# Kernel optimization log

Measured on AMD Instinct MI355X. Metric: run time of the kernel, lower is better.

Reference implementation:

```python
import jax, jax.numpy as jnp
import numpy as np

L = 3          # num_layers
D = 512        # hidden_dim
B, N = 8, 1024
EPS = 1e-5


def layernorm(x, gamma, beta):
    mu = jnp.mean(x, axis=-1, keepdims=True)
    var = jnp.var(x, axis=-1, keepdims=True)
    return (x - mu) * jax.lax.rsqrt(var + EPS) * gamma + beta


def setup_inputs() -> dict:
    key = jax.random.key(0)
    ks = jax.random.split(key, 12)
    s = 1.0 / np.sqrt(D)
    node_features = jax.random.normal(ks[0], (B, N, D), dtype=jnp.float32)
    adjacency_matrix = jax.random.randint(ks[1], (B, N, N), 0, 2, dtype=jnp.int32)
    return {
        "node_features": node_features,
        "adjacency_matrix": adjacency_matrix,
        # attn_linear: Linear(2D, 1) -> weight [2D], bias scalar, per layer
        "attn_w": jax.random.normal(ks[2], (L, 2 * D), dtype=jnp.float32) * (1.0 / np.sqrt(2 * D)),
        "attn_b": jax.random.normal(ks[3], (L,), dtype=jnp.float32) * 0.01,
        "W1": jax.random.normal(ks[4], (L, D, 4 * D), dtype=jnp.float32) * s,
        "b1": jnp.zeros((L, 4 * D), dtype=jnp.float32),
        "W2": jax.random.normal(ks[5], (L, 4 * D, D), dtype=jnp.float32) * (1.0 / np.sqrt(4 * D)),
        "b2": jnp.zeros((L, D), dtype=jnp.float32),
        "g1": jnp.ones((L, D), dtype=jnp.float32),
        "beta1": jnp.zeros((L, D), dtype=jnp.float32),
        "g2": jnp.ones((L, D), dtype=jnp.float32),
        "beta2": jnp.zeros((L, D), dtype=jnp.float32),
    }


def reference(node_features, adjacency_matrix, attn_w, attn_b, W1, b1, W2, b2, g1, beta1, g2, beta2):
    n = adjacency_matrix.shape[-1]
    # adjacency + self loops; mask of allowed edges
    mask = (adjacency_matrix.astype(jnp.float32) + jnp.eye(n, dtype=jnp.float32)) > 0  # [B,N,N]
    x = node_features
    d = x.shape[-1]
    for l in range(attn_w.shape[0]):
        # score_ij = a1.h_i + a2.h_j + b  (== Linear(concat(h_i,h_j)))
        si = x @ attn_w[l, :d]           # [B,N]
        sj = x @ attn_w[l, d:]           # [B,N]
        scores = si[:, :, None] + sj[:, None, :] + attn_b[l]   # [B,N,N]
        scores = jnp.where(scores >= 0, scores, 0.2 * scores)  # LeakyReLU(0.2)
        scores = jnp.where(mask, scores, -jnp.inf)
        attn = jax.nn.softmax(scores, axis=-1)                  # diag always unmasked
        agg = jnp.einsum('bij,bjd->bid', attn, x)
        h = layernorm(x + agg, g1[l], beta1[l])
        ff = jax.nn.gelu(h @ W1[l] + b1[l], approximate=False) @ W2[l] + b2[l]
        x = layernorm(h + ff, g2[l], beta2[l])
    return x
```

## Files before the change

### kernel.cpp

```cpp
#include <hip/hip_runtime.h>
#include <math.h>

#define NB 8
#define NN 1024
#define DD 512

typedef unsigned short u16;
typedef unsigned int u32;
typedef unsigned long long u64;
typedef __attribute__((ext_vector_type(8))) short bfrag;
typedef __attribute__((ext_vector_type(4))) float ffrag;

__device__ __forceinline__ u16 f2b(float f) {
    union { float f; u32 u; } v; v.f = f;
    u32 r = v.u + 0x7fffu + ((v.u >> 16) & 1u);
    return (u16)(r >> 16);
}
__device__ __forceinline__ float b2f(u16 b) {
    union { u32 u; float f; } v; v.u = ((u32)b) << 16;
    return v.f;
}

__device__ __forceinline__ float gelu_cheap(float v) {
    float s = v * 0.70710678118654752f;
    float a = fabsf(s);
    float t = 1.0f / (1.0f + 0.3275911f * a);
    float p = ((((1.061405429f * t - 1.453152027f) * t + 1.421413741f) * t
                - 0.284496736f) * t + 0.254829592f) * t;
    float erfa = 1.0f - p * __expf(-a * a);
    float erfs = copysignf(erfa, s);
    return 0.5f * v * (1.0f + erfs);
}

__device__ __forceinline__ void gload_lds16(const void* g, void* l) {
    __builtin_amdgcn_global_load_lds(
        (const __attribute__((address_space(1))) void*)g,
        (__attribute__((address_space(3))) void*)l, 16, 0, 0);
}

__global__ __launch_bounds__(256) void mask_pack(const int* __restrict__ adj,
                                                 u64* __restrict__ mb) {
    int idx = blockIdx.x * 256 + threadIdx.x;
    int w = idx & 15;
    int bi = idx >> 4;
    int i = bi & 1023;
    const int4* p = (const int4*)(adj + (size_t)bi * NN + w * 64);
    u64 m = 0;
#pragma unroll
    for (int q = 0; q < 16; ++q) {
        int4 v = p[q];
        if (v.x > 0) m |= 1ull << (q * 4 + 0);
        if (v.y > 0) m |= 1ull << (q * 4 + 1);
        if (v.z > 0) m |= 1ull << (q * 4 + 2);
        if (v.w > 0) m |= 1ull << (q * 4 + 3);
    }
    if (w == (i >> 6)) m |= 1ull << (i & 63);
    mb[idx] = m;
}

__global__ __launch_bounds__(256) void transpose_cvt(
    const float* __restrict__ in, u16* __restrict__ out,
    int R, int C, size_t inStr, size_t outStr)
{
    __shared__ float tile[32][33];
    int z = blockIdx.z;
    int r0 = blockIdx.y * 32, c0 = blockIdx.x * 32;
    int t = threadIdx.x;
    int tr = t >> 3, tc = (t & 7) * 4;
    float4 v = *(const float4*)(in + inStr * z + (size_t)(r0 + tr) * C + c0 + tc);
    tile[tr][tc + 0] = v.x; tile[tr][tc + 1] = v.y;
    tile[tr][tc + 2] = v.z; tile[tr][tc + 3] = v.w;
    __syncthreads();
    u32 w0 = (u32)f2b(tile[tc + 0][tr]) | ((u32)f2b(tile[tc + 1][tr]) << 16);
    u32 w1 = (u32)f2b(tile[tc + 2][tr]) | ((u32)f2b(tile[tc + 3][tr]) << 16);
    uint2 wv; wv.x = w0; wv.y = w1;
    *(uint2*)(out + outStr * z + (size_t)(c0 + tr) * R + r0 + tc) = wv;
}

__global__ __launch_bounds__(256) void score_proj_kernel(
    const float* __restrict__ x, const float* __restrict__ w,
    float* __restrict__ si, float* __restrict__ sj)
{
    int wave = threadIdx.x >> 6;
    int lane = threadIdx.x & 63;
    int row = blockIdx.x * 4 + wave;
    const float4* xr = (const float4*)(x + (size_t)row * DD) + lane * 2;
    const float4* w1 = (const float4*)(w) + lane * 2;
    const float4* w2 = (const float4*)(w + DD) + lane * 2;
    float a = 0.f, b2 = 0.f;
#pragma unroll
    for (int c = 0; c < 2; ++c) {
        float4 xv = xr[c], wa = w1[c], wb = w2[c];
        a  += xv.x * wa.x + xv.y * wa.y + xv.z * wa.z + xv.w * wa.w;
        b2 += xv.x * wb.x + xv.y * wb.y + xv.z * wb.z + xv.w * wb.w;
    }
#pragma unroll
    for (int off = 32; off > 0; off >>= 1) {
        a  += __shfl_xor(a, off);
        b2 += __shfl_xor(b2, off);
    }
    if (lane == 0) { si[row] = a; sj[row] = b2; }
}

__global__ __launch_bounds__(256) void softmax_p(
    const float* __restrict__ si, const float* __restrict__ sj,
    const float* __restrict__ attn_b, const u64* __restrict__ mb,
    u16* __restrict__ P)
{
    __shared__ u16 sb[8 * NN];
    int b  = blockIdx.x >> 7;
    int i0 = (blockIdx.x & 127) * 8;
    int tid = threadIdx.x;
    int r = tid >> 5, l32 = tid & 31;
    int i = i0 + r;
    float bb = attn_b[0];
    float siv = si[b * NN + i];
    const float* sjb = sj + b * NN;
    const u64* mbr = mb + ((size_t)b * NN + i) * 16;

    float sv[32];
    float mx = -INFINITY;
#pragma unroll
    for (int q = 0; q < 32; ++q) {
        int j = q * 32 + l32;
        u64 w = mbr[q >> 1];
        int bit = ((q & 1) << 5) + l32;
        float s = siv + sjb[j] + bb;
        s = (s >= 0.f) ? s : 0.2f * s;
        s = ((w >> bit) & 1ull) ? s : -INFINITY;
        sv[q] = s;
        mx = fmaxf(mx, s);
    }
#pragma unroll
    for (int off = 16; off > 0; off >>= 1) mx = fmaxf(mx, __shfl_xor(mx, off, 32));
    float sum = 0.f;
#pragma unroll
    for (int q = 0; q < 32; ++q) {
        float p = __expf(sv[q] - mx);
        sv[q] = p;
        sum += p;
    }
#pragma unroll
    for (int off = 16; off > 0; off >>= 1) sum += __shfl_xor(sum, off, 32);
    float inv = 1.f / sum;
#pragma unroll
    for (int q = 0; q < 32; ++q)
        sb[r * NN + q * 32 + l32] = f2b(sv[q] * inv);
    __syncthreads();
    const uint4* src = (const uint4*)sb;
    uint4* dst = (uint4*)(P + ((size_t)b * NN + i0) * NN);
#pragma unroll
    for (int t = 0; t < 4; ++t) dst[t * 256 + tid] = src[t * 256 + tid];
}

template <int EPI>
__global__ __launch_bounds__(256) void gemm64(
    const u16* __restrict__ A, const u16* __restrict__ Bm,
    const float* __restrict__ bias, const void* __restrict__ res,
    void* __restrict__ Cout, int K, int N, int lda, int ldb,
    size_t aStr, size_t bStr, size_t cStr, size_t resStr)
{
    __shared__ __align__(16) u16 lds[24576];
    int z = blockIdx.z;
    int m0 = blockIdx.y * 64, n0 = blockIdx.x * 128;
    int tid = threadIdx.x;
    int lane = tid & 63, wv = tid >> 6;

    const u16* ag[2]; const u16* bg[4];
    u32 la[2], lb[4];
#pragma unroll
    for (int i = 0; i < 2; ++i) {
        int q = i * 256 + tid;
        int row = q >> 3, c = q & 7;
        ag[i] = A + aStr * z + (size_t)(m0 + row) * lda + (c ^ (row & 7)) * 8;
        la[i] = i * 2048 + wv * 512;
    }
#pragma unroll
    for (int i = 0; i < 4; ++i) {
        int q = i * 256 + tid;
        int row = q >> 3, c = q & 7;
        bg[i] = Bm + bStr * z + (size_t)(n0 + row) * ldb + (c ^ (row & 7)) * 8;
        lb[i] = 8192 + i * 2048 + wv * 512;
    }

    int mw = (wv >> 1) * 32, nw = (wv & 1) * 64;
    int lr = lane & 15, lq = lane >> 4;
    int sw = lr & 7;

    ffrag acc[2][4];
#pragma unroll
    for (int i = 0; i < 2; ++i)
#pragma unroll
        for (int j = 0; j < 4; ++j) acc[i][j] = (ffrag){0.f, 0.f, 0.f, 0.f};

#pragma unroll
    for (int i = 0; i < 2; ++i) gload_lds16(ag[i], &lds[la[i]]);
#pragma unroll
    for (int i = 0; i < 4; ++i) gload_lds16(bg[i], &lds[lb[i]]);

    for (int k0 = 0; k0 < K; k0 += 64) {
        int cur = (k0 >> 6) & 1;
        if (k0 + 64 < K) {
#pragma unroll
            for (int i = 0; i < 2; ++i)
                gload_lds16(ag[i] + k0 + 64, &lds[((cur ^ 1) << 12) + la[i]]);
#pragma unroll
            for (int i = 0; i < 4; ++i)
                gload_lds16(bg[i] + k0 + 64, &lds[((cur ^ 1) << 13) + lb[i]]);
            asm volatile("s_waitcnt vmcnt(6)" ::: "memory");
        } else {
            asm volatile("s_waitcnt vmcnt(0)" ::: "memory");
        }
        asm volatile("s_barrier" ::: "memory");

        const u16* Ab = &lds[cur << 12];
        const u16* Bb = &lds[8192 + (cur << 13)];
#pragma unroll
        for (int h = 0; h < 2; ++h) {
            bfrag af[2], bf[4];
#pragma unroll
            for (int i = 0; i < 2; ++i)
                af[i] = *(const bfrag*)&Ab[(mw + i * 16 + lr) * 64 + ((h * 4 + lq) ^ sw) * 8];
#pragma unroll
            for (int j = 0; j < 4; ++j)
                bf[j] = *(const bfrag*)&Bb[(nw + j * 16 + lr) * 64 + ((h * 4 + lq) ^ sw) * 8];
#pragma unroll
            for (int i = 0; i < 2; ++i)
#pragma unroll
                for (int j = 0; j < 4; ++j)
                    acc[i][j] = __builtin_amdgcn_mfma_f32_16x16x32_bf16(af[i], bf[j], acc[i][j], 0, 0, 0);
        }
        asm volatile("s_waitcnt lgkmcnt(0)\ns_barrier" ::: "memory");
    }

    float* Cf = (float*)Cout + cStr * z;
    u16*   Cb = (u16*)Cout + cStr * z;
    const float* resf = (const float*)res;
    const u16*   resb = (const u16*)res;
#pragma unroll
    for (int i = 0; i < 2; ++i) {
        int row = m0 + mw + i * 16 + lq * 4;
#pragma unroll
        for (int j = 0; j < 4; ++j) {
            int col = n0 + nw + j * 16 + lr;
            float bv = (EPI != 0) ? bias[col] : 0.f;
#pragma unroll
            for (int r = 0; r < 4; ++r) {
                float v = acc[i][j][r] + bv;
                size_t off = (size_t)(row + r) * N + col;
                if (EPI == 1) {
                    Cb[off] = f2b(gelu_cheap(v));
                } else if (EPI == 0) {
                    Cf[off] = v + resf[resStr * z + off];
                } else {
                    Cf[off] = v + b2f(resb[off]);
                }
            }
        }
    }
}

template <int EPI>
__global__ __launch_bounds__(256) void gemm128(
    const u16* __restrict__ A, const u16* __restrict__ Bm,
    const float* __restrict__ bias, const void* __restrict__ res,
    void* __restrict__ Cout, int K, int N, int lda, int ldb,
    size_t aStr, size_t bStr, size_t cStr, size_t resStr)
{
    __shared__ __align__(16) u16 lds[32768];
    int z = blockIdx.z;
    int m0 = blockIdx.y * 128, n0 = blockIdx.x * 128;
    int tid = threadIdx.x;
    int lane = tid & 63, wv = tid >> 6;

    const u16* ag[4]; const u16* bg[4];
    u32 la[4], lb[4];
#pragma unroll
    for (int i = 0; i < 4; ++i) {
        int q = i * 256 + tid;
        int row = q >> 3, c = q & 7;
        ag[i] = A + aStr * z + (size_t)(m0 + row) * lda + (c ^ (row & 7)) * 8;
        la[i] = i * 2048 + wv * 512;
        bg[i] = Bm + bStr * z + (size_t)(n0 + row) * ldb + (c ^ (row & 7)) * 8;
        lb[i] = 16384 + i * 2048 + wv * 512;
    }

    int mw = (wv >> 1) * 64, nw = (wv & 1) * 64;
    int lr = lane & 15, lq = lane >> 4;
    int sw = lr & 7;

    ffrag acc[4][4];
#pragma unroll
    for (int i = 0; i < 4; ++i)
#pragma unroll
        for (int j = 0; j < 4; ++j) acc[i][j] = (ffrag){0.f, 0.f, 0.f, 0.f};

#pragma unroll
    for (int i = 0; i < 4; ++i) gload_lds16(ag[i], &lds[la[i]]);
#pragma unroll
    for (int i = 0; i < 4; ++i) gload_lds16(bg[i], &lds[lb[i]]);

    for (int k0 = 0; k0 < K; k0 += 64) {
        int cur = (k0 >> 6) & 1;
        if (k0 + 64 < K) {
#pragma unroll
            for (int i = 0; i < 4; ++i)
                gload_lds16(ag[i] + k0 + 64, &lds[((cur ^ 1) << 13) + la[i]]);
#pragma unroll
            for (int i = 0; i < 4; ++i)
                gload_lds16(bg[i] + k0 + 64, &lds[((cur ^ 1) << 13) + lb[i]]);
            asm volatile("s_waitcnt vmcnt(8)" ::: "memory");
        } else {
            asm volatile("s_waitcnt vmcnt(0)" ::: "memory");
        }
        asm volatile("s_barrier" ::: "memory");

        const u16* Ab = &lds[cur << 13];
        const u16* Bb = &lds[16384 + (cur << 13)];
#pragma unroll
        for (int h = 0; h < 2; ++h) {
            bfrag af[4], bf[4];
#pragma unroll
            for (int i = 0; i < 4; ++i)
                af[i] = *(const bfrag*)&Ab[(mw + i * 16 + lr) * 64 + ((h * 4 + lq) ^ sw) * 8];
#pragma unroll
            for (int j = 0; j < 4; ++j)
                bf[j] = *(const bfrag*)&Bb[(nw + j * 16 + lr) * 64 + ((h * 4 + lq) ^ sw) * 8];
#pragma unroll
            for (int i = 0; i < 4; ++i)
#pragma unroll
                for (int j = 0; j < 4; ++j)
                    acc[i][j] = __builtin_amdgcn_mfma_f32_16x16x32_bf16(af[i], bf[j], acc[i][j], 0, 0, 0);
        }
        asm volatile("s_waitcnt lgkmcnt(0)\ns_barrier" ::: "memory");
    }

    float* Cf = (float*)Cout + cStr * z;
    u16*   Cb = (u16*)Cout + cStr * z;
    const float* resf = (const float*)res;
    const u16*   resb = (const u16*)res;
#pragma unroll
    for (int i = 0; i < 4; ++i) {
        int row = m0 + mw + i * 16 + lq * 4;
#pragma unroll
        for (int j = 0; j < 4; ++j) {
            int col = n0 + nw + j * 16 + lr;
            float bv = (EPI != 0) ? bias[col] : 0.f;
#pragma unroll
            for (int r = 0; r < 4; ++r) {
                float v = acc[i][j][r] + bv;
                size_t off = (size_t)(row + r) * N + col;
                if (EPI == 1) {
                    Cb[off] = f2b(gelu_cheap(v));
                } else if (EPI == 0) {
                    Cf[off] = v + resf[resStr * z + off];
                } else {
                    Cf[off] = v + b2f(resb[off]);
                }
            }
        }
    }
}

template <bool BF, bool SP>
__global__ __launch_bounds__(256) void ln_kernel(
    const float* __restrict__ in, const float* __restrict__ g,
    const float* __restrict__ be, void* __restrict__ out,
    const float* __restrict__ aw, float* __restrict__ si, float* __restrict__ sj)
{
    int row = blockIdx.x;
    int tid = threadIdx.x;
    const float2* rp = (const float2*)(in + (size_t)row * DD);
    float2 v = rp[tid];
    float s  = v.x + v.y;
    float ss = v.x * v.x + v.y * v.y;
#pragma unroll
    for (int off = 32; off > 0; off >>= 1) {
        s  += __shfl_xor(s, off);
        ss += __shfl_xor(ss, off);
    }
    __shared__ float sh[8];
    int wave = tid >> 6, lane = tid & 63;
    if (lane == 0) { sh[wave] = s; sh[4 + wave] = ss; }
    __syncthreads();
    float S  = sh[0] + sh[1] + sh[2] + sh[3];
    float SS = sh[4] + sh[5] + sh[6] + sh[7];
    float mean = S * (1.f / DD);
    float var  = SS * (1.f / DD) - mean * mean;
    var = fmaxf(var, 0.f);
    float rs = rsqrtf(var + 1e-5f);
    float2 gv = ((const float2*)g)[tid];
    float2 bv = ((const float2*)be)[tid];
    float ox = (v.x - mean) * rs * gv.x + bv.x;
    float oy = (v.y - mean) * rs * gv.y + bv.y;
    if (BF) {
        u32 w = (u32)f2b(ox) | ((u32)f2b(oy) << 16);
        ((u32*)out)[(size_t)row * (DD / 2) + tid] = w;
    } else {
        float2 o; o.x = ox; o.y = oy;
        ((float2*)out)[(size_t)row * (DD / 2) + tid] = o;
    }
    if (SP) {
        float2 wa = ((const float2*)aw)[tid];
        float2 wb = ((const float2*)(aw + DD))[tid];
        float a = ox * wa.x + oy * wa.y;
        float c = ox * wb.x + oy * wb.y;
#pragma unroll
        for (int off = 32; off > 0; off >>= 1) {
            a += __shfl_xor(a, off);
            c += __shfl_xor(c, off);
        }
        __syncthreads();
        if (lane == 0) { sh[wave] = a; sh[4 + wave] = c; }
        __syncthreads();
        if (tid == 0) {
            si[row] = sh[0] + sh[1] + sh[2] + sh[3];
            sj[row] = sh[4] + sh[5] + sh[6] + sh[7];
        }
    }
}

extern "C" void kernel_launch(void* const* d_in, const int* in_sizes, int n_in,
                              void* d_out, int out_size, void* d_ws, size_t ws_size,
                              hipStream_t stream) {
    const float* nf     = (const float*)d_in[0];
    const int*   adj    = (const int*)d_in[1];
    const float* attn_w = (const float*)d_in[2];
    const float* attn_b = (const float*)d_in[3];
    const float* W1     = (const float*)d_in[4];
    const float* b1     = (const float*)d_in[5];
    const float* W2     = (const float*)d_in[6];
    const float* b2     = (const float*)d_in[7];
    const float* g1     = (const float*)d_in[8];
    const float* be1    = (const float*)d_in[9];
    const float* g2     = (const float*)d_in[10];
    const float* be2    = (const float*)d_in[11];
    float* out = (float*)d_out;

    char* wsb = (char*)d_ws;
    float* x_cur = (float*)(wsb);
    u16*   h_bf  = (u16*)(wsb + 16777216);
    char*  scr   = wsb + 25165824;
    u16*   P     = (u16*)scr;
    float* hres  = (float*)(scr + 16777216);
    u16*   mid   = (u16*)scr;
    u16*   xT    = (u16*)(wsb + 58720256);
    u16*   W1t   = (u16*)(wsb + 67108864);
    u16*   W2t   = (u16*)(wsb + 73400320);
    u64*   mask  = (u64*)(wsb + 79691776);
    float* si    = (float*)(wsb + 80740352);
    float* sj    = (float*)(wsb + 80773120);

    mask_pack<<<512, 256, 0, stream>>>(adj, mask);
    transpose_cvt<<<dim3(64, 16, 3), 256, 0, stream>>>(W1, W1t, 512, 2048,
                                                       (size_t)512 * 2048, (size_t)512 * 2048);
    transpose_cvt<<<dim3(16, 64, 3), 256, 0, stream>>>(W2, W2t, 2048, 512,
                                                       (size_t)2048 * 512, (size_t)2048 * 512);

    score_proj_kernel<<<2048, 256, 0, stream>>>(nf, attn_w, si, sj);

    for (int l = 0; l < 3; ++l) {
        const float* xin = (l == 0) ? nf : x_cur;
        transpose_cvt<<<dim3(16, 32, 8), 256, 0, stream>>>(xin, xT, 1024, 512,
                                                           (size_t)NN * DD, (size_t)NN * DD);
        softmax_p<<<1024, 256, 0, stream>>>(si, sj, attn_b + l, mask, P);
        gemm64<0><<<dim3(4, 16, 8), 256, 0, stream>>>(
            P, xT, nullptr, xin, hres, 1024, 512, 1024, 1024,
            (size_t)NN * NN, (size_t)DD * NN, (size_t)NN * DD, (size_t)NN * DD);
        ln_kernel<true, false><<<8192, 256, 0, stream>>>(
            hres, g1 + (size_t)l * 512, be1 + (size_t)l * 512, h_bf, nullptr, nullptr, nullptr);
        gemm128<1><<<dim3(16, 64, 1), 256, 0, stream>>>(
            h_bf, W1t + (size_t)l * 1048576, b1 + (size_t)l * 2048, nullptr, mid,
            512, 2048, 512, 512, 0, 0, 0, 0);
        gemm64<2><<<dim3(4, 128, 1), 256, 0, stream>>>(
            mid, W2t + (size_t)l * 1048576, b2 + (size_t)l * 512, h_bf, x_cur,
            2048, 512, 2048, 2048, 0, 0, 0, 0);
        if (l < 2) {
            ln_kernel<false, true><<<8192, 256, 0, stream>>>(
                x_cur, g2 + (size_t)l * 512, be2 + (size_t)l * 512, x_cur,
                attn_w + (size_t)(l + 1) * 1024, si, sj);
        } else {
            ln_kernel<false, false><<<8192, 256, 0, stream>>>(
                x_cur, g2 + (size_t)l * 512, be2 + (size_t)l * 512, out,
                nullptr, nullptr, nullptr);
        }
    }
}
```

Measured before the change: 476.0 us.

## Remap GEMM workgroups across XCDs and stage GELU epilogue stores through LDS

Both GEMM kernels now remap the linear workgroup index so that consecutive tiles land on the same XCD (stride-8 interleave), which should improve L2 reuse of shared A/B panels on the chiplet GPU. The GELU epilogue of gemm128 writes bf16 results into LDS with a padded stride, then copies them out as coalesced 16-byte row stores instead of scattered 2-byte stores. The remap assumes the workgroup count is divisible by 8, and the LDS staging adds a barrier.

```diff
diff --git a/kernel.cpp b/kernel.cpp
--- a/kernel.cpp
+++ b/kernel.cpp
@@ -161,8 +161,14 @@
     size_t aStr, size_t bStr, size_t cStr, size_t resStr)
 {
     __shared__ __align__(16) u16 lds[24576];
-    int z = blockIdx.z;
-    int m0 = blockIdx.y * 64, n0 = blockIdx.x * 128;
+    int gx = gridDim.x, gy = gridDim.y;
+    int wg = blockIdx.x + gx * (blockIdx.y + gy * blockIdx.z);
+    int nwg = gx * gy * gridDim.z;
+    wg = (wg & 7) * (nwg >> 3) + (wg >> 3);
+    int z = wg / (gx * gy);
+    int rem = wg - z * (gx * gy);
+    int by = rem / gx, bx = rem - by * gx;
+    int m0 = by * 64, n0 = bx * 128;
     int tid = threadIdx.x;
     int lane = tid & 63, wv = tid >> 6;
 
@@ -268,8 +274,14 @@
     size_t aStr, size_t bStr, size_t cStr, size_t resStr)
 {
     __shared__ __align__(16) u16 lds[32768];
-    int z = blockIdx.z;
-    int m0 = blockIdx.y * 128, n0 = blockIdx.x * 128;
+    int gx = gridDim.x, gy = gridDim.y;
+    int wg = blockIdx.x + gx * (blockIdx.y + gy * blockIdx.z);
+    int nwg = gx * gy * gridDim.z;
+    wg = (wg & 7) * (nwg >> 3) + (wg >> 3);
+    int z = wg / (gx * gy);
+    int rem = wg - z * (gx * gy);
+    int by = rem / gx, bx = rem - by * gx;
+    int m0 = by * 128, n0 = bx * 128;
     int tid = threadIdx.x;
     int lane = tid & 63, wv = tid >> 6;
 
@@ -339,23 +351,46 @@
     u16*   Cb = (u16*)Cout + cStr * z;
     const float* resf = (const float*)res;
     const u16*   resb = (const u16*)res;
-#pragma unroll
-    for (int i = 0; i < 4; ++i) {
-        int row = m0 + mw + i * 16 + lq * 4;
-#pragma unroll
-        for (int j = 0; j < 4; ++j) {
-            int col = n0 + nw + j * 16 + lr;
-            float bv = (EPI != 0) ? bias[col] : 0.f;
-#pragma unroll
-            for (int r = 0; r < 4; ++r) {
-                float v = acc[i][j][r] + bv;
-                size_t off = (size_t)(row + r) * N + col;
-                if (EPI == 1) {
-                    Cb[off] = f2b(gelu_cheap(v));
-                } else if (EPI == 0) {
-                    Cf[off] = v + resf[resStr * z + off];
-                } else {
-                    Cf[off] = v + b2f(resb[off]);
+    if (EPI == 1) {
+        u16* sb = lds;
+#pragma unroll
+        for (int i = 0; i < 4; ++i) {
+            int rr = mw + i * 16 + lq * 4;
+#pragma unroll
+            for (int j = 0; j < 4; ++j) {
+                int cc = nw + j * 16 + lr;
+                float bv = bias[n0 + cc];
+#pragma unroll
+                for (int r = 0; r < 4; ++r)
+                    sb[(rr + r) * 136 + cc] = f2b(gelu_cheap(acc[i][j][r] + bv));
+            }
+        }
+        __syncthreads();
+        u16* Crow = Cb + (size_t)m0 * N + n0;
+#pragma unroll
+        for (int t = 0; t < 8; ++t) {
+            int q = t * 256 + tid;
+            int row = q >> 4, c16 = q & 15;
+            *(uint4*)(Crow + (size_t)row * N + c16 * 8) =
+                *(const uint4*)(sb + row * 136 + c16 * 8);
+        }
+    } else {
+#pragma unroll
+        for (int i = 0; i < 4; ++i) {
+            int row = m0 + mw + i * 16 + lq * 4;
+#pragma unroll
+            for (int j = 0; j < 4; ++j) {
+                int col = n0 + nw + j * 16 + lr;
+                float bv = (EPI != 0) ? bias[col] : 0.f;
+#pragma unroll
+                for (int r = 0; r < 4; ++r) {
+                    float v = acc[i][j][r] + bv;
+                    size_t off = (size_t)(row + r) * N + col;
+                    if (EPI == 0) {
+                        Cf[off] = v + resf[resStr * z + off];
+                    } else {
+                        Cf[off] = v + b2f(resb[off]);
+                    }
                 }
             }
         }
```

New measurement: 454.9 us. 4.4% less time.
